# Kernel optimization log

Hardware: AMD Instinct MI355X
Metric: run time of the kernel (lower is better)

The kernel has to match this reference:

```python
import jax, jax.numpy as jnp
import numpy as np


def _entropy(x):
    # x: [..., C]; rowwise entropy of softmax(x) along last axis
    logp = jax.nn.log_softmax(x, axis=-1)
    return -(jnp.exp(logp) * logp).sum(-1)


def setup_inputs() -> dict:
    key = jax.random.key(0)
    C, E = 8192, 512
    prototypes = jax.random.normal(key, (C, E), dtype=jnp.float32)
    return {"prototypes": prototypes}


def reference(prototypes):
    C, E = prototypes.shape
    # F.normalize(p=2, dim=1): divide by L2 norm clamped to 1e-12
    norm = jnp.sqrt(jnp.sum(prototypes * prototypes, axis=1, keepdims=True))
    p = prototypes / jnp.maximum(norm, 1e-12)
    # Gram matrix [C, C] (fused matmul instead of broadcast-mul-sum)
    proto_logits = jnp.einsum("ce,de->cd", p, p)
    proto_logits_sum = proto_logits.sum(0, keepdims=True)  # [1, C]
    loss = _entropy(proto_logits).sum(-1) / C + _entropy(proto_logits_sum)
    return loss.sum()
```

## Files before the change

### kernel.cpp

```cpp
#include <hip/hip_runtime.h>
#include <hip/hip_bf16.h>

#define C_DIM 8192
#define E_DIM 512

using f32x4 = __attribute__((ext_vector_type(4))) float;
using i32x4 = __attribute__((ext_vector_type(4))) int;

__device__ inline void gload_lds16(const void* g, void* l) {
  __builtin_amdgcn_global_load_lds(
      (const __attribute__((address_space(1))) unsigned*)g,
      (__attribute__((address_space(3))) unsigned*)l, 16, 0, 0);
}

__device__ inline unsigned pack_bf16(float a, float b) {
  unsigned ua = __float_as_uint(a), ub = __float_as_uint(b);
  ua = (ua + 0x7fffu + ((ua >> 16) & 1u)) >> 16;
  ub = (ub + 0x7fffu + ((ub >> 16) & 1u)) >> 16;
  return ua | (ub << 16);
}

__device__ inline float bf2f(unsigned short u) {
  return __uint_as_float(((unsigned)u) << 16);
}

__device__ inline unsigned pack_i8x4(float a, float b, float c, float d) {
  unsigned x0 = (unsigned)(__float2int_rn(a * 127.f)) & 255u;
  unsigned x1 = (unsigned)(__float2int_rn(b * 127.f)) & 255u;
  unsigned x2 = (unsigned)(__float2int_rn(c * 127.f)) & 255u;
  unsigned x3 = (unsigned)(__float2int_rn(d * 127.f)) & 255u;
  return x0 | (x1 << 8) | (x2 << 16) | (x3 << 24);
}

__global__ __launch_bounds__(256) void norm_kernel(
    const float* __restrict__ P, unsigned* __restrict__ Pb,
    unsigned* __restrict__ Pi, float* __restrict__ q,
    float* __restrict__ h_acc, unsigned* __restrict__ done) {
  if (blockIdx.x == 0) {
    int t = threadIdx.x;
    q[t] = 0.f;
    q[t + 256] = 0.f;
    if (t == 0) { h_acc[0] = 0.f; done[0] = 0u; }
  }
  int wid = threadIdx.x >> 6, lane = threadIdx.x & 63;
  int row = blockIdx.x * 4 + wid;
  const float4* src = (const float4*)(P + (size_t)row * E_DIM);
  float4 v0 = src[lane], v1 = src[lane + 64];
  float ss = v0.x * v0.x + v0.y * v0.y + v0.z * v0.z + v0.w * v0.w +
             v1.x * v1.x + v1.y * v1.y + v1.z * v1.z + v1.w * v1.w;
  for (int m = 32; m; m >>= 1) ss += __shfl_xor(ss, m);
  float inv = 1.0f / fmaxf(sqrtf(ss), 1e-12f);
  v0.x *= inv; v0.y *= inv; v0.z *= inv; v0.w *= inv;
  v1.x *= inv; v1.y *= inv; v1.z *= inv; v1.w *= inv;
  uint2* bd = (uint2*)(Pb + (size_t)row * (E_DIM / 2));
  uint2 b0, b1;
  b0.x = pack_bf16(v0.x, v0.y); b0.y = pack_bf16(v0.z, v0.w);
  b1.x = pack_bf16(v1.x, v1.y); b1.y = pack_bf16(v1.z, v1.w);
  bd[lane] = b0; bd[lane + 64] = b1;
  Pi[(size_t)row * 128 + lane] = pack_i8x4(v0.x, v0.y, v0.z, v0.w);
  Pi[(size_t)row * 128 + 64 + lane] = pack_i8x4(v1.x, v1.y, v1.z, v1.w);
}

__global__ __launch_bounds__(256) void qsum_kernel(
    const unsigned short* __restrict__ Pb, float* __restrict__ q) {
  __shared__ float red[4][512];
  int wid = threadIdx.x >> 6, lane = threadIdx.x & 63;
  float a[8];
#pragma unroll
  for (int k = 0; k < 8; ++k) a[k] = 0.f;
  for (int i = 0; i < 32; ++i) {
    int row = blockIdx.x * 128 + wid * 32 + i;
    uint4 v = *(const uint4*)(Pb + (size_t)row * E_DIM + lane * 8);
    a[0] += bf2f((unsigned short)(v.x & 0xffff));
    a[1] += bf2f((unsigned short)(v.x >> 16));
    a[2] += bf2f((unsigned short)(v.y & 0xffff));
    a[3] += bf2f((unsigned short)(v.y >> 16));
    a[4] += bf2f((unsigned short)(v.z & 0xffff));
    a[5] += bf2f((unsigned short)(v.z >> 16));
    a[6] += bf2f((unsigned short)(v.w & 0xffff));
    a[7] += bf2f((unsigned short)(v.w >> 16));
  }
#pragma unroll
  for (int k = 0; k < 8; ++k) red[wid][lane * 8 + k] = a[k];
  __syncthreads();
  for (int c = threadIdx.x; c < 512; c += 256) {
    float t = red[0][c] + red[1][c] + red[2][c] + red[3][c];
    atomicAdd(&q[c], t);
  }
}

__global__ __launch_bounds__(256) void ssum_kernel(
    const unsigned short* __restrict__ Pb, const float* __restrict__ q,
    float* __restrict__ s) {
  int wid = threadIdx.x >> 6, lane = threadIdx.x & 63;
  int row = blockIdx.x * 4 + wid;
  uint4 v = *(const uint4*)(Pb + (size_t)row * E_DIM + lane * 8);
  const float4* qv = (const float4*)q;
  float4 q0 = qv[lane * 2], q1 = qv[lane * 2 + 1];
  float d = bf2f((unsigned short)(v.x & 0xffff)) * q0.x +
            bf2f((unsigned short)(v.x >> 16)) * q0.y +
            bf2f((unsigned short)(v.y & 0xffff)) * q0.z +
            bf2f((unsigned short)(v.y >> 16)) * q0.w +
            bf2f((unsigned short)(v.z & 0xffff)) * q1.x +
            bf2f((unsigned short)(v.z >> 16)) * q1.y +
            bf2f((unsigned short)(v.w & 0xffff)) * q1.z +
            bf2f((unsigned short)(v.w >> 16)) * q1.w;
  for (int m = 32; m; m >>= 1) d += __shfl_xor(d, m);
  if (lane == 0) s[row] = d;
}

__global__ __launch_bounds__(256, 3) void gram_kernel(
    const unsigned char* __restrict__ Pi, float* __restrict__ Zp,
    float* __restrict__ Sp) {
  __shared__ unsigned char As[128 * 128];
  __shared__ unsigned char Bs[128 * 128];

  int b = blockIdx.x;
  int i = (b & 7) * 260 + (b >> 3);
  float bi = 64.5f - sqrtf(64.5f * 64.5f - 2.0f * (float)i);
  int by = (int)bi;
  if (by < 0) by = 0;
  while (64 * (by + 1) - ((by + 1) * by) / 2 <= i) ++by;
  while (64 * by - (by * (by - 1)) / 2 > i) --by;
  int bx = by + (i - (64 * by - (by * (by - 1)) / 2));
  bool diag = (bx == by);

  int tid = threadIdx.x, wid = tid >> 6, lane = tid & 63;
  int wr = wid >> 1, wc = wid & 1;
  int l15 = lane & 15, lh = lane >> 4;

  i32x4 acc[4][4];
#pragma unroll
  for (int m = 0; m < 4; ++m)
#pragma unroll
    for (int n = 0; n < 4; ++n)
      acc[m][n] = (i32x4){0, 0, 0, 0};

  int rs = lane >> 3;
  int gsw = (lane & 7) ^ rs;
  const unsigned char* abase = Pi + (size_t)(by * 128) * E_DIM;
  const unsigned char* bbase = Pi + (size_t)(bx * 128) * E_DIM;

  for (int kt = 0; kt < 4; ++kt) {
#pragma unroll
    for (int j = 0; j < 4; ++j) {
      int ci = wid * 4 + j;
      int r = ci * 8 + rs;
      gload_lds16(abase + (size_t)r * E_DIM + kt * 128 + gsw * 16,
                  (char*)As + ci * 1024);
      gload_lds16(bbase + (size_t)r * E_DIM + kt * 128 + gsw * 16,
                  (char*)Bs + ci * 1024);
    }
    __syncthreads();

#pragma unroll
    for (int kk = 0; kk < 2; ++kk) {
      i32x4 af[4], bfr[4];
#pragma unroll
      for (int m = 0; m < 4; ++m) {
        int row = wr * 64 + m * 16 + l15;
        int g = (kk * 4 + lh) ^ (row & 7);
        af[m] = *(const i32x4*)(As + row * 128 + g * 16);
      }
#pragma unroll
      for (int n = 0; n < 4; ++n) {
        int row = wc * 64 + n * 16 + l15;
        int g = (kk * 4 + lh) ^ (row & 7);
        bfr[n] = *(const i32x4*)(Bs + row * 128 + g * 16);
      }
#pragma unroll
      for (int m = 0; m < 4; ++m)
#pragma unroll
        for (int n = 0; n < 4; ++n)
          acc[m][n] = __builtin_amdgcn_mfma_i32_16x16x64_i8(
              af[m], bfr[n], acc[m][n], 0, 0, 0);
    }
    if (kt < 3) __syncthreads();
  }

  const float invq = 1.0f / 16129.0f;
  float zc[4], sc[4];
#pragma unroll
  for (int n = 0; n < 4; ++n) { zc[n] = 0.f; sc[n] = 0.f; }

  int slotR = bx * 2 + wc;
#pragma unroll
  for (int m = 0; m < 4; ++m) {
#pragma unroll
    for (int reg = 0; reg < 4; ++reg) {
      float z = 0.f, s = 0.f;
#pragma unroll
      for (int n = 0; n < 4; ++n) {
        float g = (float)acc[m][n][reg] * invq;
        float e = __expf(g);
        z += e;
        s += e * g;
        zc[n] += e;
        sc[n] += e * g;
      }
      for (int msk = 8; msk; msk >>= 1) {
        z += __shfl_xor(z, msk);
        s += __shfl_xor(s, msk);
      }
      if (l15 == 0) {
        int rowin = wr * 64 + m * 16 + lh * 4 + reg;
        size_t idx = (size_t)by * 16384 + (size_t)slotR * 128 + rowin;
        Zp[idx] = z;
        Sp[idx] = s;
      }
    }
  }
  if (!diag) {
    int slotC = by * 2 + wr;
#pragma unroll
    for (int n = 0; n < 4; ++n) {
      float z = zc[n], s = sc[n];
      z += __shfl_xor(z, 16); s += __shfl_xor(s, 16);
      z += __shfl_xor(z, 32); s += __shfl_xor(s, 32);
      if (lh == 0) {
        int colin = wc * 64 + n * 16 + l15;
        size_t idx = (size_t)bx * 16384 + (size_t)slotC * 128 + colin;
        Zp[idx] = z;
        Sp[idx] = s;
      }
    }
  }
}

__global__ __launch_bounds__(256) void reduce_kernel(
    const float* __restrict__ Zp, const float* __restrict__ Sp,
    const float* __restrict__ s, float* __restrict__ h_acc,
    unsigned* __restrict__ done, float* __restrict__ out) {
  __shared__ float zbuf[128], sbuf[128];
  __shared__ float red[8];
  __shared__ unsigned lastFlag;
  int rb = blockIdx.x;
  int t = threadIdx.x;
  int lane = t & 63, wid = t >> 6;
  int row = t & 127;
  const float* src = (t >= 128) ? Sp : Zp;
  size_t base = (size_t)rb * 16384 + row;
  float acc = 0.f;
#pragma unroll 8
  for (int sl = 0; sl < 128; ++sl) acc += src[base + (size_t)sl * 128];
  if (t >= 128) sbuf[row] = acc; else zbuf[row] = acc;
  __syncthreads();

  float hp = 0.f;
  if (t < 128) {
    float z = zbuf[t], s2 = sbuf[t];
    hp = logf(z) - s2 / z;
  }
  for (int k = 32; k; k >>= 1) hp += __shfl_xor(hp, k);
  if (lane == 0) red[wid] = hp;
  __syncthreads();
  if (t == 0) {
    float h = red[0] + red[1];
    atomicAdd(h_acc, h);
    __threadfence();
    unsigned old = atomicAdd(done, 1u);
    lastFlag = (old == 63u) ? 1u : 0u;
  }
  __syncthreads();

  if (lastFlag) {
    float m = -3.4e38f;
    for (int i = t; i < C_DIM; i += 256) m = fmaxf(m, s[i]);
    for (int k = 32; k; k >>= 1) m = fmaxf(m, __shfl_xor(m, k));
    if (lane == 0) red[wid] = m;
    __syncthreads();
    m = fmaxf(fmaxf(red[0], red[1]), fmaxf(red[2], red[3]));

    float z = 0.f, sw = 0.f;
    for (int i = t; i < C_DIM; i += 256) {
      float tv = s[i] - m;
      float e = __expf(tv);
      z += e;
      sw += e * tv;
    }
    for (int k = 32; k; k >>= 1) {
      z += __shfl_xor(z, k);
      sw += __shfl_xor(sw, k);
    }
    __syncthreads();
    if (lane == 0) { red[wid] = z; red[4 + wid] = sw; }
    __syncthreads();
    if (t == 0) {
      float zt = red[0] + red[1] + red[2] + red[3];
      float st = red[4] + red[5] + red[6] + red[7];
      float H2 = logf(zt) - st / zt;
      float h = atomicAdd(h_acc, 0.0f);
      out[0] = h / (float)C_DIM + H2;
    }
  }
}

extern "C" void kernel_launch(void* const* d_in, const int* in_sizes, int n_in,
                              void* d_out, int out_size, void* d_ws, size_t ws_size,
                              hipStream_t stream) {
  const float* P = (const float*)d_in[0];
  float* out = (float*)d_out;

  char* ws = (char*)d_ws;
  unsigned* Pb = (unsigned*)ws;
  unsigned* Pi = (unsigned*)(ws + ((size_t)8 << 20));
  float* Zp = (float*)(ws + ((size_t)12 << 20));
  float* Sp = (float*)(ws + ((size_t)16 << 20));
  float* q = (float*)(ws + ((size_t)20 << 20));
  float* h_acc = (float*)(ws + ((size_t)20 << 20) + 2048);
  unsigned* done = (unsigned*)(ws + ((size_t)20 << 20) + 2052);
  float* s = (float*)(ws + ((size_t)20 << 20) + 4096);

  norm_kernel<<<C_DIM / 4, 256, 0, stream>>>(P, Pb, Pi, q, h_acc, done);
  qsum_kernel<<<C_DIM / 128, 256, 0, stream>>>((const unsigned short*)Pb, q);
  ssum_kernel<<<C_DIM / 4, 256, 0, stream>>>((const unsigned short*)Pb, q, s);
  gram_kernel<<<2080, 256, 0, stream>>>((const unsigned char*)Pi, Zp, Sp);
  reduce_kernel<<<64, 256, 0, stream>>>(Zp, Sp, s, h_acc, done, out);
}
```

Before: 73.69 us.

## Fuse qsum and ssum via grid barrier; compact gram partial slots through LDS

```diff
diff --git a/kernel.cpp b/kernel.cpp
--- a/kernel.cpp
+++ b/kernel.cpp
@@ -35,12 +35,13 @@
 __global__ __launch_bounds__(256) void norm_kernel(
     const float* __restrict__ P, unsigned* __restrict__ Pb,
     unsigned* __restrict__ Pi, float* __restrict__ q,
-    float* __restrict__ h_acc, unsigned* __restrict__ done) {
+    float* __restrict__ h_acc, unsigned* __restrict__ done,
+    unsigned* __restrict__ qdone) {
   if (blockIdx.x == 0) {
     int t = threadIdx.x;
     q[t] = 0.f;
     q[t + 256] = 0.f;
-    if (t == 0) { h_acc[0] = 0.f; done[0] = 0u; }
+    if (t == 0) { h_acc[0] = 0.f; done[0] = 0u; qdone[0] = 0u; }
   }
   int wid = threadIdx.x >> 6, lane = threadIdx.x & 63;
   int row = blockIdx.x * 4 + wid;
@@ -61,8 +62,9 @@
   Pi[(size_t)row * 128 + 64 + lane] = pack_i8x4(v1.x, v1.y, v1.z, v1.w);
 }
 
-__global__ __launch_bounds__(256) void qsum_kernel(
-    const unsigned short* __restrict__ Pb, float* __restrict__ q) {
+__global__ __launch_bounds__(256) void qsum_ssum_kernel(
+    const unsigned short* __restrict__ Pb, float* __restrict__ q,
+    unsigned* __restrict__ qdone, float* __restrict__ s) {
   __shared__ float red[4][512];
   int wid = threadIdx.x >> 6, lane = threadIdx.x & 63;
   float a[8];
@@ -87,26 +89,37 @@
     float t = red[0][c] + red[1][c] + red[2][c] + red[3][c];
     atomicAdd(&q[c], t);
   }
-}
-
-__global__ __launch_bounds__(256) void ssum_kernel(
-    const unsigned short* __restrict__ Pb, const float* __restrict__ q,
-    float* __restrict__ s) {
-  int wid = threadIdx.x >> 6, lane = threadIdx.x & 63;
-  int row = blockIdx.x * 4 + wid;
-  uint4 v = *(const uint4*)(Pb + (size_t)row * E_DIM + lane * 8);
-  const float4* qv = (const float4*)q;
-  float4 q0 = qv[lane * 2], q1 = qv[lane * 2 + 1];
-  float d = bf2f((unsigned short)(v.x & 0xffff)) * q0.x +
-            bf2f((unsigned short)(v.x >> 16)) * q0.y +
-            bf2f((unsigned short)(v.y & 0xffff)) * q0.z +
-            bf2f((unsigned short)(v.y >> 16)) * q0.w +
-            bf2f((unsigned short)(v.z & 0xffff)) * q1.x +
-            bf2f((unsigned short)(v.z >> 16)) * q1.y +
-            bf2f((unsigned short)(v.w & 0xffff)) * q1.z +
-            bf2f((unsigned short)(v.w >> 16)) * q1.w;
-  for (int m = 32; m; m >>= 1) d += __shfl_xor(d, m);
-  if (lane == 0) s[row] = d;
+  __syncthreads();
+
+  if (threadIdx.x == 0) {
+    __threadfence();
+    __hip_atomic_fetch_add(qdone, 1u, __ATOMIC_RELEASE, __HIP_MEMORY_SCOPE_AGENT);
+    while (__hip_atomic_load(qdone, __ATOMIC_ACQUIRE, __HIP_MEMORY_SCOPE_AGENT) <
+           64u)
+      __builtin_amdgcn_s_sleep(2);
+  }
+  __syncthreads();
+
+  float qreg[8];
+#pragma unroll
+  for (int k = 0; k < 8; ++k)
+    qreg[k] = __hip_atomic_load(&q[lane * 8 + k], __ATOMIC_RELAXED,
+                                __HIP_MEMORY_SCOPE_AGENT);
+
+  for (int i = 0; i < 32; ++i) {
+    int row = blockIdx.x * 128 + wid * 32 + i;
+    uint4 v = *(const uint4*)(Pb + (size_t)row * E_DIM + lane * 8);
+    float d = bf2f((unsigned short)(v.x & 0xffff)) * qreg[0] +
+              bf2f((unsigned short)(v.x >> 16)) * qreg[1] +
+              bf2f((unsigned short)(v.y & 0xffff)) * qreg[2] +
+              bf2f((unsigned short)(v.y >> 16)) * qreg[3] +
+              bf2f((unsigned short)(v.z & 0xffff)) * qreg[4] +
+              bf2f((unsigned short)(v.z >> 16)) * qreg[5] +
+              bf2f((unsigned short)(v.w & 0xffff)) * qreg[6] +
+              bf2f((unsigned short)(v.w >> 16)) * qreg[7];
+    for (int m = 32; m; m >>= 1) d += __shfl_xor(d, m);
+    if (lane == 0) s[row] = d;
+  }
 }
 
 __global__ __launch_bounds__(256, 3) void gram_kernel(
@@ -178,12 +191,15 @@
     if (kt < 3) __syncthreads();
   }
 
+  __syncthreads();
+  float* zb = (float*)As;
+  float* sb = (float*)Bs;
+
   const float invq = 1.0f / 16129.0f;
   float zc[4], sc[4];
 #pragma unroll
   for (int n = 0; n < 4; ++n) { zc[n] = 0.f; sc[n] = 0.f; }
 
-  int slotR = bx * 2 + wc;
 #pragma unroll
   for (int m = 0; m < 4; ++m) {
 #pragma unroll
@@ -198,20 +214,29 @@
         zc[n] += e;
         sc[n] += e * g;
       }
-      for (int msk = 8; msk; msk >>= 1) {
-        z += __shfl_xor(z, msk);
-        s += __shfl_xor(s, msk);
-      }
-      if (l15 == 0) {
-        int rowin = wr * 64 + m * 16 + lh * 4 + reg;
-        size_t idx = (size_t)by * 16384 + (size_t)slotR * 128 + rowin;
-        Zp[idx] = z;
-        Sp[idx] = s;
-      }
-    }
-  }
+      int row = wr * 64 + m * 16 + lh * 4 + reg;
+      int gph = (wc * 4 + (l15 >> 2)) ^ (row & 7);
+      int idx = row * 32 + gph * 4 + (l15 & 3);
+      zb[idx] = z;
+      sb[idx] = s;
+    }
+  }
+  __syncthreads();
+
+  {
+    int r = tid & 127;
+    const float* buf = (tid >= 128) ? sb : zb;
+    f32x4 a = {0.f, 0.f, 0.f, 0.f};
+#pragma unroll
+    for (int g = 0; g < 8; ++g) a += *(const f32x4*)(buf + r * 32 + g * 4);
+    float tot = a[0] + a[1] + a[2] + a[3];
+    int slotR = bx - by;
+    size_t idx = (size_t)by * 16384 + (size_t)slotR * 128 + r;
+    if (tid >= 128) Sp[idx] = tot; else Zp[idx] = tot;
+  }
+
   if (!diag) {
-    int slotC = by * 2 + wr;
+    int slotC = (64 - bx) + 2 * by + wr;
 #pragma unroll
     for (int n = 0; n < 4; ++n) {
       float z = zc[n], s = sc[n];
@@ -241,8 +266,9 @@
   const float* src = (t >= 128) ? Sp : Zp;
   size_t base = (size_t)rb * 16384 + row;
   float acc = 0.f;
-#pragma unroll 8
-  for (int sl = 0; sl < 128; ++sl) acc += src[base + (size_t)sl * 128];
+  int nsl = 64 + rb;
+#pragma unroll 4
+  for (int sl = 0; sl < nsl; ++sl) acc += src[base + (size_t)sl * 128];
   if (t >= 128) sbuf[row] = acc; else zbuf[row] = acc;
   __syncthreads();
 
@@ -309,11 +335,11 @@
   float* q = (float*)(ws + ((size_t)20 << 20));
   float* h_acc = (float*)(ws + ((size_t)20 << 20) + 2048);
   unsigned* done = (unsigned*)(ws + ((size_t)20 << 20) + 2052);
+  unsigned* qdone = (unsigned*)(ws + ((size_t)20 << 20) + 2056);
   float* s = (float*)(ws + ((size_t)20 << 20) + 4096);
 
-  norm_kernel<<<C_DIM / 4, 256, 0, stream>>>(P, Pb, Pi, q, h_acc, done);
-  qsum_kernel<<<C_DIM / 128, 256, 0, stream>>>((const unsigned short*)Pb, q);
-  ssum_kernel<<<C_DIM / 4, 256, 0, stream>>>((const unsigned short*)Pb, q, s);
+  norm_kernel<<<C_DIM / 4, 256, 0, stream>>>(P, Pb, Pi, q, h_acc, done, qdone);
+  qsum_ssum_kernel<<<64, 256, 0, stream>>>((const unsigned short*)Pb, q, qdone, s);
   gram_kernel<<<2080, 256, 0, stream>>>((const unsigned char*)Pi, Zp, Sp);
   reduce_kernel<<<64, 256, 0, stream>>>(Zp, Sp, s, h_acc, done, out);
 }
```

Result: slower. 86.31 us (+17.1%).

## Reduce row partials in LDS and compact the partial-sum slot layout

Applied to the files above, without the earlier changes.

```diff
diff --git a/kernel.cpp b/kernel.cpp
--- a/kernel.cpp
+++ b/kernel.cpp
@@ -178,12 +178,15 @@
     if (kt < 3) __syncthreads();
   }
 
+  __syncthreads();
+  float* zb = (float*)As;
+  float* sb = (float*)Bs;
+
   const float invq = 1.0f / 16129.0f;
   float zc[4], sc[4];
 #pragma unroll
   for (int n = 0; n < 4; ++n) { zc[n] = 0.f; sc[n] = 0.f; }
 
-  int slotR = bx * 2 + wc;
 #pragma unroll
   for (int m = 0; m < 4; ++m) {
 #pragma unroll
@@ -198,20 +201,30 @@
         zc[n] += e;
         sc[n] += e * g;
       }
-      for (int msk = 8; msk; msk >>= 1) {
-        z += __shfl_xor(z, msk);
-        s += __shfl_xor(s, msk);
-      }
-      if (l15 == 0) {
-        int rowin = wr * 64 + m * 16 + lh * 4 + reg;
-        size_t idx = (size_t)by * 16384 + (size_t)slotR * 128 + rowin;
-        Zp[idx] = z;
-        Sp[idx] = s;
-      }
-    }
-  }
+      int row = wr * 64 + m * 16 + lh * 4 + reg;
+      int gph = (wc * 4 + (l15 >> 2)) ^ (row & 7);
+      int idx = row * 32 + gph * 4 + (l15 & 3);
+      zb[idx] = z;
+      sb[idx] = s;
+    }
+  }
+  __syncthreads();
+
+  {
+    int r = tid & 127;
+    const float* buf = (tid >= 128) ? sb : zb;
+    f32x4 a = {0.f, 0.f, 0.f, 0.f};
+#pragma unroll
+    for (int g = 0; g < 8; ++g)
+      a += *(const f32x4*)(buf + r * 32 + ((g ^ (r & 7)) * 4));
+    float tot = a[0] + a[1] + a[2] + a[3];
+    int slotR = bx - by;
+    size_t idx = (size_t)by * 16384 + (size_t)slotR * 128 + r;
+    if (tid >= 128) Sp[idx] = tot; else Zp[idx] = tot;
+  }
+
   if (!diag) {
-    int slotC = by * 2 + wr;
+    int slotC = (64 - bx) + 2 * by + wr;
 #pragma unroll
     for (int n = 0; n < 4; ++n) {
       float z = zc[n], s = sc[n];
@@ -241,8 +254,9 @@
   const float* src = (t >= 128) ? Sp : Zp;
   size_t base = (size_t)rb * 16384 + row;
   float acc = 0.f;
-#pragma unroll 8
-  for (int sl = 0; sl < 128; ++sl) acc += src[base + (size_t)sl * 128];
+  int nsl = 64 + rb;
+#pragma unroll 4
+  for (int sl = 0; sl < nsl; ++sl) acc += src[base + (size_t)sl * 128];
   if (t >= 128) sbuf[row] = acc; else zbuf[row] = acc;
   __syncthreads();
 
```

Result: faster. 70.59 us (-4.2%).
